# Performance work log

Measured on AMD Instinct MI355X. Metric: run time of the kernel, lower is better.

Reference implementation:

```python
import jax, jax.numpy as jnp
import numpy as np

B, C_IN, H, W = 8, 64, 224, 224
C_OUT, HID = 64, 64
KH = KW = 3
IN_SZ = C_IN * KH * KW  # 576, unfold feature size (c, kh, kw order)


def setup_inputs() -> dict:
    key = jax.random.key(0)
    k_x, k_w1, k_b1, k_w2, k_b2 = jax.random.split(key, 5)
    bound1 = 1.0 / np.sqrt(IN_SZ)
    bound2 = 1.0 / np.sqrt(HID)
    return {
        "x": jax.random.normal(k_x, (B, C_IN, H, W), dtype=jnp.float32),
        "W1": jax.random.uniform(k_w1, (HID, IN_SZ), jnp.float32, -bound1, bound1),
        "b1": jax.random.uniform(k_b1, (HID,), jnp.float32, -bound1, bound1),
        "W2": jax.random.uniform(k_w2, (C_OUT, HID), jnp.float32, -bound2, bound2),
        "b2": jax.random.uniform(k_b2, (C_OUT,), jnp.float32, -bound2, bound2),
    }


def reference(x, W1, b1, W2, b2):
    # First Linear over unfold patches == implicit-GEMM conv: W1 rows are
    # flattened (c, kh, kw) exactly matching F.unfold's feature ordering.
    w_conv = W1.reshape(HID, C_IN, KH, KW)
    h = jax.lax.conv_general_dilated(
        x, w_conv,
        window_strides=(1, 1),
        padding=((1, 1), (1, 1)),
        rhs_dilation=(1, 1),
        dimension_numbers=("NCHW", "OIHW", "NCHW"),
    ) + b1[None, :, None, None]
    h = jax.nn.relu(h)
    # Second Linear acts per patch location == pointwise (1x1) contraction.
    out = jnp.einsum("bchw,oc->bohw", h, W2) + b2[None, :, None, None]
    return out
```

## Files before the change

kernel.cpp:

```cpp
#include <hip/hip_runtime.h>

typedef __attribute__((ext_vector_type(8))) short bf16x8;
typedef __attribute__((ext_vector_type(4))) float f32x4;

static constexpr int HH = 224, WW = 224;
static constexpr int CIN = 64;

__device__ __forceinline__ ushort f2bf(float f) {
    unsigned u = __builtin_bit_cast(unsigned, f);
    u += 0x7FFFu + ((u >> 16) & 1u);
    return (ushort)(u >> 16);
}

__global__ void prep_kernel(const float* __restrict__ W1, const float* __restrict__ W2,
                            ushort* __restrict__ w1r, ushort* __restrict__ w2r) {
    const int idx = blockIdx.x * 256 + threadIdx.x;
    if (idx < 36864) {
        const int ch = idx >> 12;
        const int n = (idx >> 6) & 63;
        const int c = idx & 63;
        w1r[idx] = f2bf(W1[n * 576 + c * 9 + ch]);
    } else if (idx < 40960) {
        const int j = idx - 36864;
        w2r[j] = f2bf(W2[j]);
    }
}

__global__ __launch_bounds__(256, 3)
void mlpconv_kernel(const float* __restrict__ xin, const ushort* __restrict__ w1r,
                    const float* __restrict__ b1, const ushort* __restrict__ w2r,
                    const float* __restrict__ b2, float* __restrict__ out) {
    __shared__ ushort xs[10 * 40 * 64];

    const int tid = threadIdx.x;
    const int wave = tid >> 6;
    const int lane = tid & 63;
    const int l15 = lane & 15;
    const int quad = lane >> 4;

    const int x0 = blockIdx.x * 32;
    const int y0 = blockIdx.y * 8;
    const int b = blockIdx.z;

    const float* xg = xin + (size_t)b * (CIN * HH * WW);

    for (int e = tid; e < 6400; e += 256) {
        const int i = e % 10;
        const int t = e / 10;
        const int c = t & 63;
        const int r = t >> 6;
        const int gy = y0 + r - 1;
        const int gx4 = x0 - 4 + i * 4;
        float4 v = make_float4(0.f, 0.f, 0.f, 0.f);
        if (((unsigned)gy < (unsigned)HH) && ((unsigned)gx4 <= 220u))
            v = *reinterpret_cast<const float4*>(xg + (c * HH + gy) * WW + gx4);
        const int p0 = r * 40 + i * 4;
        xs[(p0 + 0) * 64 + (c ^ (((p0 + 0) & 7) * 8))] = f2bf(v.x);
        xs[(p0 + 1) * 64 + (c ^ (((p0 + 1) & 7) * 8))] = f2bf(v.y);
        xs[(p0 + 2) * 64 + (c ^ (((p0 + 2) & 7) * 8))] = f2bf(v.z);
        xs[(p0 + 3) * 64 + (c ^ (((p0 + 3) & 7) * 8))] = f2bf(v.w);
    }

    float b1v[4];
    #pragma unroll
    for (int nt = 0; nt < 4; ++nt) b1v[nt] = b1[nt * 16 + l15];

    f32x4 acc[4][4];
    #pragma unroll
    for (int mt = 0; mt < 4; ++mt)
        #pragma unroll
        for (int nt = 0; nt < 4; ++nt)
            acc[mt][nt] = (f32x4){b1v[nt], b1v[nt], b1v[nt], b1v[nt]};

    __syncthreads();

    #pragma unroll 2
    for (int ks = 0; ks < 18; ++ks) {
        const int ch = ks >> 1;
        const int s = ks & 1;
        const int dy = ch / 3, dx = ch - 3 * (ch / 3);
        const int ko = s * 32 + quad * 8;
        bf16x8 bfr[4];
        #pragma unroll
        for (int nt = 0; nt < 4; ++nt)
            bfr[nt] = *reinterpret_cast<const bf16x8*>(
                w1r + ch * 4096 + (nt * 16 + l15) * 64 + ko);
        const int kswz = ko ^ (((l15 + dx + 3) & 7) * 8);
        #pragma unroll
        for (int mt = 0; mt < 4; ++mt) {
            const int row = 2 * wave + (mt >> 1) + dy;
            const int col = (mt & 1) * 16 + l15 + dx + 3;
            const bf16x8 afr = *reinterpret_cast<const bf16x8*>(
                &xs[(row * 40 + col) * 64 + kswz]);
            #pragma unroll
            for (int nt = 0; nt < 4; ++nt)
                acc[mt][nt] = __builtin_amdgcn_mfma_f32_16x16x32_bf16(
                    afr, bfr[nt], acc[mt][nt], 0, 0, 0);
        }
    }

    __syncthreads();

    float4 b2q[4];
    #pragma unroll
    for (int it = 0; it < 4; ++it)
        b2q[it] = *reinterpret_cast<const float4*>(b2 + it * 16 + quad * 4);

    bf16x8 wa2[2][4];
    #pragma unroll
    for (int k2 = 0; k2 < 2; ++k2)
        #pragma unroll
        for (int it = 0; it < 4; ++it)
            wa2[k2][it] = *reinterpret_cast<const bf16x8*>(
                w2r + (it * 16 + l15) * 64 + k2 * 32 + quad * 8);

    ushort* myh = &xs[wave * (16 * 72)];
    float* outg = out + (size_t)b * (64 * HH * WW);

    #pragma unroll
    for (int mt = 0; mt < 4; ++mt) {
        #pragma unroll
        for (int ni = 0; ni < 4; ++ni)
            #pragma unroll
            for (int r = 0; r < 4; ++r) {
                float v = acc[mt][ni][r];
                v = v > 0.f ? v : 0.f;
                myh[(quad * 4 + r) * 72 + ni * 16 + l15] = f2bf(v);
            }
        f32x4 acc2[4];
        #pragma unroll
        for (int it = 0; it < 4; ++it)
            acc2[it] = (f32x4){b2q[it].x, b2q[it].y, b2q[it].z, b2q[it].w};
        #pragma unroll
        for (int k2 = 0; k2 < 2; ++k2) {
            const bf16x8 hb = *reinterpret_cast<const bf16x8*>(
                &myh[l15 * 72 + k2 * 32 + quad * 8]);
            #pragma unroll
            for (int it = 0; it < 4; ++it)
                acc2[it] = __builtin_amdgcn_mfma_f32_16x16x32_bf16(
                    wa2[k2][it], hb, acc2[it], 0, 0, 0);
        }
        const int gy = y0 + 2 * wave + (mt >> 1);
        const int gx = x0 + (mt & 1) * 16 + l15;
        #pragma unroll
        for (int it = 0; it < 4; ++it)
            #pragma unroll
            for (int r = 0; r < 4; ++r) {
                const int o = it * 16 + quad * 4 + r;
                outg[(o * HH + gy) * WW + gx] = acc2[it][r];
            }
    }
}

extern "C" void kernel_launch(void* const* d_in, const int* in_sizes, int n_in,
                              void* d_out, int out_size, void* d_ws, size_t ws_size,
                              hipStream_t stream) {
    const float* x  = (const float*)d_in[0];
    const float* W1 = (const float*)d_in[1];
    const float* b1 = (const float*)d_in[2];
    const float* W2 = (const float*)d_in[3];
    const float* b2 = (const float*)d_in[4];
    float* out = (float*)d_out;

    ushort* w1r = (ushort*)d_ws;
    ushort* w2r = w1r + 9 * 64 * 64;

    prep_kernel<<<160, 256, 0, stream>>>(W1, W2, w1r, w2r);
    dim3 grid(WW / 32, HH / 8, 8);
    mlpconv_kernel<<<grid, dim3(256), 0, stream>>>(x, w1r, b1, w2r, b2, out);
}
```

Measured before the change: 289.3 us.

## Pre-transpose input to NHWC bf16 and stage tiles via direct global-to-LDS loads

Adds a separate kernel that converts x from NCHW fp32 to an NHWC bf16 copy in workspace. The main kernel then fills its LDS halo tile with global_load_lds 16-byte transfers, using a zero page for padding, in place of per-element fp32 loads, bf16 conversion and scattered swizzled LDS stores. The aim is to cut the staging cost inside the conv kernel. In exchange it adds an extra full pass over the input (an fp32 read plus a bf16 write) and an extra kernel launch, and it only runs when the workspace is large enough.

```diff
diff --git a/kernel.cpp b/kernel.cpp
--- a/kernel.cpp
+++ b/kernel.cpp
@@ -5,6 +5,7 @@
 
 static constexpr int HH = 224, WW = 224;
 static constexpr int CIN = 64;
+static constexpr int HW = HH * WW;
 
 __device__ __forceinline__ ushort f2bf(float f) {
     unsigned u = __builtin_bit_cast(unsigned, f);
@@ -13,16 +14,166 @@
 }
 
 __global__ void prep_kernel(const float* __restrict__ W1, const float* __restrict__ W2,
-                            ushort* __restrict__ w1r, ushort* __restrict__ w2r) {
+                            ushort* __restrict__ ws, int nfill) {
     const int idx = blockIdx.x * 256 + threadIdx.x;
     if (idx < 36864) {
         const int ch = idx >> 12;
         const int n = (idx >> 6) & 63;
         const int c = idx & 63;
-        w1r[idx] = f2bf(W1[n * 576 + c * 9 + ch]);
+        ws[idx] = f2bf(W1[n * 576 + c * 9 + ch]);
     } else if (idx < 40960) {
-        const int j = idx - 36864;
-        w2r[j] = f2bf(W2[j]);
+        ws[idx] = f2bf(W2[idx - 36864]);
+    } else if (idx < nfill) {
+        ws[idx] = 0;
+    }
+}
+
+__global__ __launch_bounds__(256)
+void xprep_kernel(const float* __restrict__ xin, ushort* __restrict__ xt) {
+    const int b = blockIdx.y;
+    const float* xg = xin + (size_t)b * (CIN * HW);
+    ushort* xo = xt + (size_t)b * ((size_t)HW * 64);
+    const int base = blockIdx.x * 1024 + threadIdx.x;
+    #pragma unroll
+    for (int it = 0; it < 4; ++it) {
+        const int idx = base + it * 256;
+        const int p = ((idx >> 9) << 6) | (idx & 63);
+        const int cg = (idx >> 6) & 7;
+        bf16x8 o;
+        #pragma unroll
+        for (int j = 0; j < 8; ++j)
+            o[j] = (short)f2bf(xg[(cg * 8 + j) * HW + p]);
+        *reinterpret_cast<bf16x8*>(xo + (size_t)p * 64 + cg * 8) = o;
+    }
+}
+
+#define GLD_LDS16(g, l) __builtin_amdgcn_global_load_lds(                  \
+    (const __attribute__((address_space(1))) void*)(g),                    \
+    (__attribute__((address_space(3))) void*)(l), 16, 0, 0)
+
+__global__ __launch_bounds__(256, 3)
+void mlpconv_fast(const ushort* __restrict__ xt, const ushort* __restrict__ w1r,
+                  const float* __restrict__ b1, const ushort* __restrict__ w2r,
+                  const float* __restrict__ b2, const ushort* __restrict__ zp,
+                  float* __restrict__ out) {
+    __shared__ ushort xs[10 * 40 * 64];
+
+    const int tid = threadIdx.x;
+    const int wave = tid >> 6;
+    const int lane = tid & 63;
+    const int l15 = lane & 15;
+    const int quad = lane >> 4;
+
+    const int x0 = blockIdx.x * 32;
+    const int y0 = blockIdx.y * 8;
+    const int b = blockIdx.z;
+
+    const ushort* xtb = xt + (size_t)b * ((size_t)HW * 64);
+
+    const int lpx = lane >> 3;
+    const int laneoff = lpx * 64 + (((lane & 7) ^ lpx) * 8);
+
+    for (int q = wave; q < 50; q += 4) {
+        const int r = q / 5;
+        const int i = q - 5 * r;
+        const int gy = y0 + r - 1;
+        const int gx0 = x0 - 4 + i * 8;
+        const ushort* real = xtb + (long)(gy * WW + gx0) * 64 + laneoff;
+        const bool ok = ((unsigned)gy < (unsigned)HH) &
+                        ((unsigned)(gx0 + lpx) < (unsigned)WW);
+        const ushort* src = ok ? real : zp;
+        GLD_LDS16(src, &xs[(r * 40 + i * 8) * 64]);
+    }
+
+    float b1v[4];
+    #pragma unroll
+    for (int nt = 0; nt < 4; ++nt) b1v[nt] = b1[nt * 16 + l15];
+
+    f32x4 acc[4][4];
+    #pragma unroll
+    for (int mt = 0; mt < 4; ++mt)
+        #pragma unroll
+        for (int nt = 0; nt < 4; ++nt)
+            acc[mt][nt] = (f32x4){b1v[nt], b1v[nt], b1v[nt], b1v[nt]};
+
+    asm volatile("s_waitcnt vmcnt(0)" ::: "memory");
+    __syncthreads();
+
+    #pragma unroll 2
+    for (int ks = 0; ks < 18; ++ks) {
+        const int ch = ks >> 1;
+        const int s = ks & 1;
+        const int dy = ch / 3, dx = ch - 3 * (ch / 3);
+        const int ko = s * 32 + quad * 8;
+        bf16x8 bfr[4];
+        #pragma unroll
+        for (int nt = 0; nt < 4; ++nt)
+            bfr[nt] = *reinterpret_cast<const bf16x8*>(
+                w1r + ch * 4096 + (nt * 16 + l15) * 64 + ko);
+        const int kswz = ko ^ (((l15 + dx + 3) & 7) * 8);
+        #pragma unroll
+        for (int mt = 0; mt < 4; ++mt) {
+            const int row = 2 * wave + (mt >> 1) + dy;
+            const int col = (mt & 1) * 16 + l15 + dx + 3;
+            const bf16x8 afr = *reinterpret_cast<const bf16x8*>(
+                &xs[(row * 40 + col) * 64 + kswz]);
+            #pragma unroll
+            for (int nt = 0; nt < 4; ++nt)
+                acc[mt][nt] = __builtin_amdgcn_mfma_f32_16x16x32_bf16(
+                    afr, bfr[nt], acc[mt][nt], 0, 0, 0);
+        }
+    }
+
+    __syncthreads();
+
+    float4 b2q[4];
+    #pragma unroll
+    for (int it = 0; it < 4; ++it)
+        b2q[it] = *reinterpret_cast<const float4*>(b2 + it * 16 + quad * 4);
+
+    bf16x8 wa2[2][4];
+    #pragma unroll
+    for (int k2 = 0; k2 < 2; ++k2)
+        #pragma unroll
+        for (int it = 0; it < 4; ++it)
+            wa2[k2][it] = *reinterpret_cast<const bf16x8*>(
+                w2r + (it * 16 + l15) * 64 + k2 * 32 + quad * 8);
+
+    ushort* myh = &xs[wave * (16 * 72)];
+    float* outg = out + (size_t)b * (64 * HH * WW);
+
+    #pragma unroll
+    for (int mt = 0; mt < 4; ++mt) {
+        #pragma unroll
+        for (int ni = 0; ni < 4; ++ni)
+            #pragma unroll
+            for (int r = 0; r < 4; ++r) {
+                float v = acc[mt][ni][r];
+                v = v > 0.f ? v : 0.f;
+                myh[(quad * 4 + r) * 72 + ni * 16 + l15] = f2bf(v);
+            }
+        f32x4 acc2[4];
+        #pragma unroll
+        for (int it = 0; it < 4; ++it)
+            acc2[it] = (f32x4){b2q[it].x, b2q[it].y, b2q[it].z, b2q[it].w};
+        #pragma unroll
+        for (int k2 = 0; k2 < 2; ++k2) {
+            const bf16x8 hb = *reinterpret_cast<const bf16x8*>(
+                &myh[l15 * 72 + k2 * 32 + quad * 8]);
+            #pragma unroll
+            for (int it = 0; it < 4; ++it)
+                acc2[it] = __builtin_amdgcn_mfma_f32_16x16x32_bf16(
+                    wa2[k2][it], hb, acc2[it], 0, 0, 0);
+        }
+        const int gy = y0 + 2 * wave + (mt >> 1);
+        const int gx = x0 + (mt & 1) * 16 + l15;
+        #pragma unroll
+        for (int it = 0; it < 4; ++it)
+            #pragma unroll
+            for (int r = 0; r < 4; ++r) {
+                const int o = it * 16 + quad * 4 + r;
+                outg[(o * HH + gy) * WW + gx] = acc2[it][r];
+            }
     }
 }
 
@@ -162,10 +313,21 @@
     const float* b2 = (const float*)d_in[4];
     float* out = (float*)d_out;
 
-    ushort* w1r = (ushort*)d_ws;
-    ushort* w2r = w1r + 9 * 64 * 64;
-
-    prep_kernel<<<160, 256, 0, stream>>>(W1, W2, w1r, w2r);
+    ushort* ws  = (ushort*)d_ws;
+    ushort* w1r = ws;
+    ushort* w2r = ws + 36864;
+    ushort* zp  = ws + 40960;
+    ushort* xt  = ws + 41024;
+
+    const size_t need = (size_t)41024 * 2 + (size_t)8 * HW * 64 * 2;
+    const bool fast = ws_size >= need;
+
+    prep_kernel<<<161, 256, 0, stream>>>(W1, W2, ws, fast ? 41024 : 40960);
     dim3 grid(WW / 32, HH / 8, 8);
-    mlpconv_kernel<<<grid, dim3(256), 0, stream>>>(x, w1r, b1, w2r, b2, out);
-}
+    if (fast) {
+        xprep_kernel<<<dim3(392, 8), 256, 0, stream>>>(x, xt);
+        mlpconv_fast<<<grid, dim3(256), 0, stream>>>(xt, w1r, b1, w2r, b2, zp, out);
+    } else {
+        mlpconv_kernel<<<grid, dim3(256), 0, stream>>>(x, w1r, b1, w2r, b2, out);
+    }
+}
```

New measurement: 302.3 us. 4.5% more time.
